# Kernel optimization log

Hardware: AMD Instinct MI355X
Metric: run time of the kernel (lower is better)

Reference implementation:

```python
import math
import jax, jax.numpy as jnp
import numpy as np

NQ, NK = 16384, 4096
QDIM, KDIM, MID = 512, 256, 256


def setup_inputs() -> dict:
    key = jax.random.key(0)
    k1, k2, k3, k4, k5, k6, k7, k8 = jax.random.split(key, 8)
    return {
        "global_embeddings": jax.random.normal(k1, (NQ, QDIM), dtype=jnp.float32),
        "substruct_embeddings": jax.random.normal(k2, (NK, KDIM), dtype=jnp.float32),
        "substruct_weight": jax.random.uniform(k3, (NK,), dtype=jnp.float32),
        "mask": jax.random.randint(k4, (NQ, NK), 0, 2, dtype=jnp.int32),
        "Wq": jax.random.normal(k5, (MID, QDIM), dtype=jnp.float32) / math.sqrt(QDIM),
        "bq": jax.random.normal(k6, (MID,), dtype=jnp.float32) * 0.01,
        "Wk": jax.random.normal(k7, (MID, KDIM), dtype=jnp.float32) / math.sqrt(KDIM),
        "bk": jax.random.normal(k8, (MID,), dtype=jnp.float32) * 0.01,
    }


def reference(global_embeddings, substruct_embeddings, substruct_weight, mask, Wq, bq, Wk, bk):
    # Q/K projections (torch Linear: x @ W.T + b)
    Q = global_embeddings @ Wq.T + bq            # [NQ, MID]
    K = substruct_embeddings @ Wk.T + bk         # [NK, MID]
    scores = (Q @ K.T) / math.sqrt(MID)          # [NQ, NK]
    scores = jnp.where(mask == 0, -jnp.inf, scores)
    attn = jax.nn.softmax(scores, axis=-1)       # row-wise stable softmax
    # torch.diag(w) @ E  ==  elementwise row scaling
    V = substruct_weight[:, None] * substruct_embeddings  # [NK, KDIM]
    return attn @ V                              # [NQ, KDIM]
```

## Files before the change

kernel.cpp:

```cpp
#include <hip/hip_runtime.h>
#include <hip/hip_bf16.h>

typedef __bf16 bf16_t;
typedef bf16_t bf16x8 __attribute__((ext_vector_type(8)));
typedef float  f32x4  __attribute__((ext_vector_type(4)));
typedef unsigned long long u64;
typedef unsigned int u32;

#define MFMA16(A,B,C) __builtin_amdgcn_mfma_f32_16x16x32_bf16((A),(B),(C),0,0,0)


static __device__ __forceinline__ void gl_lds16(const bf16_t* g, void* l) {
    __builtin_amdgcn_global_load_lds(
        (const __attribute__((address_space(1))) u32*)(const void*)g,
        (__attribute__((address_space(3))) u32*)l, 16, 0, 0);
}

template<int KA, bool SWZ>
__global__ __launch_bounds__(256)
void proj_kernel(const float* __restrict__ A, const float* __restrict__ W,
                 const float* __restrict__ b, bf16_t* __restrict__ C,
                 float scale)
{
    __shared__ bf16_t Alds[64][40];
    __shared__ bf16_t Wlds[256][40];

    const int t  = threadIdx.x;
    const int w  = t >> 6, l = t & 63, lr = l & 15, lg = l >> 4;
    const int m0 = blockIdx.x * 64;

    f32x4 acc[16];
#pragma unroll
    for (int tt = 0; tt < 16; ++tt) acc[tt] = (f32x4){0.f, 0.f, 0.f, 0.f};

    const int ar  = t >> 2;
    const int ac8 = (t & 3) * 8;

    for (int kb = 0; kb < KA / 32; ++kb) {
        {
            const float* ap = A + (size_t)(m0 + ar) * KA + kb * 32 + ac8;
            float4 a0 = *(const float4*)ap;
            float4 a1 = *(const float4*)(ap + 4);
            bf16x8 av;
            av[0]=(bf16_t)a0.x; av[1]=(bf16_t)a0.y; av[2]=(bf16_t)a0.z; av[3]=(bf16_t)a0.w;
            av[4]=(bf16_t)a1.x; av[5]=(bf16_t)a1.y; av[6]=(bf16_t)a1.z; av[7]=(bf16_t)a1.w;
            *(bf16x8*)&Alds[ar][ac8] = av;
        }
#pragma unroll
        for (int c = 0; c < 4; ++c) {
            int e8 = c * 256 + t;
            int wr = e8 >> 2, wc8 = (e8 & 3) * 8;
            const float* wp = W + (size_t)wr * KA + kb * 32 + wc8;
            float4 w0 = *(const float4*)wp;
            float4 w1 = *(const float4*)(wp + 4);
            bf16x8 wv;
            wv[0]=(bf16_t)w0.x; wv[1]=(bf16_t)w0.y; wv[2]=(bf16_t)w0.z; wv[3]=(bf16_t)w0.w;
            wv[4]=(bf16_t)w1.x; wv[5]=(bf16_t)w1.y; wv[6]=(bf16_t)w1.z; wv[7]=(bf16_t)w1.w;
            *(bf16x8*)&Wlds[wr][wc8] = wv;
        }
        __syncthreads();

        bf16x8 af = *(bf16x8*)&Alds[w * 16 + lr][lg * 8];
#pragma unroll
        for (int tt = 0; tt < 16; ++tt) {
            bf16x8 bfrag = *(bf16x8*)&Wlds[tt * 16 + lr][lg * 8];
            acc[tt] = MFMA16(af, bfrag, acc[tt]);
        }
        __syncthreads();
    }

#pragma unroll
    for (int tt = 0; tt < 16; ++tt) {
        int col = tt * 16 + lr;
        float bias = b[col];
#pragma unroll
        for (int r = 0; r < 4; ++r) {
            int row = m0 + w * 16 + lg * 4 + r;
            int colS = col;
            if (SWZ) colS = (((col >> 3) ^ (row & 7)) << 3) | (col & 7);
            C[(size_t)row * 256 + colS] = (bf16_t)((acc[tt][r] + bias) * scale);
        }
    }
}

__global__ __launch_bounds__(256)
void buildvt_kernel(const float* __restrict__ S, const float* __restrict__ wgt,
                    bf16_t* __restrict__ VT)
{
    int i = blockIdx.x * 256 + threadIdx.x;
    int d = i >> 12, k = i & 4095;
    int kt = (k & ~63) | (((((k >> 3) & 7) ^ (d & 7)) << 3)) | (k & 7);
    VT[i] = (bf16_t)(wgt[kt] * S[(size_t)kt * 256 + d]);
}

template<bool SPLIT>
__global__ __launch_bounds__(512, 2)
void attn_kernel(const bf16_t* __restrict__ Qb, const bf16_t* __restrict__ Kb,
                 const bf16_t* __restrict__ VT, const int* __restrict__ mask,
                 float* __restrict__ out, float* __restrict__ pacc,
                 float* __restrict__ pm, float* __restrict__ pl)
{
    __shared__ __align__(16) char Kraw[2][32768];
    __shared__ __align__(16) char Vraw[2][32768];
    __shared__ __align__(16) char Praw[16384];

    const int t  = threadIdx.x;
    const int w  = t >> 6, l = t & 63, lr = l & 15, lg = l >> 4;
    const int qw = blockIdx.x * 128 + w * 16;
    const int half = SPLIT ? (int)blockIdx.y : 0;
    const int NT   = SPLIT ? 32 : 64;
    const int kb0  = half * NT;

    bf16x8 qf[8];
    {
        const bf16_t* qrow = Qb + (size_t)(qw + lr) * 256;
#pragma unroll
        for (int kk = 0; kk < 8; ++kk)
            qf[kk] = *(const bf16x8*)(qrow + kk * 32 + lg * 8);
    }

    bf16x8 vone;
#pragma unroll
    for (int j = 0; j < 8; ++j) vone[j] = (bf16_t)1.0f;

    f32x4 acc[16];
#pragma unroll
    for (int dt = 0; dt < 16; ++dt) acc[dt] = (f32x4){0.f, 0.f, 0.f, 0.f};
    f32x4 lacc = (f32x4){0.f, 0.f, 0.f, 0.f};
    float mrow[4];
#pragma unroll
    for (int r = 0; r < 4; ++r) mrow[r] = -1e30f;

    auto stage = [&](int kb, char* kd, char* vd) {
#pragma unroll
        for (int i = 0; i < 4; ++i) {
            int row = w * 8 + i * 2 + (l >> 5);
            gl_lds16(Kb + (size_t)(kb * 64 + row) * 256 + (l & 31) * 8,
                     kd + (w * 8 + i * 2) * 512);
        }
#pragma unroll
        for (int i = 0; i < 4; ++i) {
            int d = w * 32 + i * 8 + (l >> 3);
            gl_lds16(VT + (size_t)d * 4096 + kb * 64 + (l & 7) * 8,
                     vd + (w * 32 + i * 8) * 128);
        }
    };

    auto iter = [&](int kb, char* kcur, char* vcur, char* knxt, char* vnxt,
                    bool do_stage) {
        int4 mv[4];
#pragma unroll
        for (int r = 0; r < 4; ++r)
            mv[r] = *(const int4*)(mask + (size_t)(qw + 4 * lg + r) * 4096
                                   + kb * 64 + lr * 4);

        if (do_stage) stage(kb + 1, knxt, vnxt);

        u64 rowbits[4];
#pragma unroll
        for (int r = 0; r < 4; ++r) {
            u64 b0 = __ballot(mv[r].x != 0);
            u64 b1 = __ballot(mv[r].y != 0);
            u64 b2 = __ballot(mv[r].z != 0);
            u64 b3 = __ballot(mv[r].w != 0);
            u64 w01  = (lr & 1) ? b1 : b0;
            u64 w23  = (lr & 1) ? b3 : b2;
            u64 wsel = (lr & 2) ? w23 : w01;
            rowbits[r] = wsel >> (lg * 16 + (lr >> 2));
        }

        f32x4 s[4];
#pragma unroll
        for (int tt = 0; tt < 4; ++tt) {
            f32x4 sv = (f32x4){0.f, 0.f, 0.f, 0.f};
#pragma unroll
            for (int kk = 0; kk < 8; ++kk) {
                bf16x8 kf = *(bf16x8*)(kcur + (((tt * 16 + lr) * 512)
                                | ((((kk * 4 + lg) ^ (lr & 7)) << 4))));
                sv = MFMA16(qf[kk], kf, sv);
            }
            s[tt] = sv;
        }
#pragma unroll
        for (int tt = 0; tt < 4; ++tt)
#pragma unroll
            for (int r = 0; r < 4; ++r) {
                bool keep = ((rowbits[r] >> (4 * tt)) & 1ull) != 0;
                s[tt][r] = keep ? s[tt][r] : -1e30f;
            }

        float bm[4];
#pragma unroll
        for (int r = 0; r < 4; ++r)
            bm[r] = fmaxf(fmaxf(s[0][r], s[1][r]), fmaxf(s[2][r], s[3][r]));
#pragma unroll
        for (int off = 1; off < 16; off <<= 1)
#pragma unroll
            for (int r = 0; r < 4; ++r)
                bm[r] = fmaxf(bm[r], __shfl_xor(bm[r], off));

        bool need = false;
#pragma unroll
        for (int r = 0; r < 4; ++r) need = need || (bm[r] > mrow[r] + 8.f);
        if (__any(need)) {
#pragma unroll
            for (int r = 0; r < 4; ++r) {
                float mn = fmaxf(mrow[r], bm[r]);
                float fr = __expf(mrow[r] - mn);
                mrow[r] = mn;
                lacc[r] *= fr;
#pragma unroll
                for (int dt = 0; dt < 16; ++dt) acc[dt][r] *= fr;
            }
        }

#pragma unroll
        for (int tt = 0; tt < 4; ++tt)
#pragma unroll
            for (int r = 0; r < 4; ++r) {
                int prow = w * 16 + lg * 4 + r;
                *(bf16_t*)(Praw + ((prow * 128 + (tt * 16 + lr) * 2)
                                   ^ ((prow & 7) << 4)))
                    = (bf16_t)__expf(s[tt][r] - mrow[r]);
            }
        asm volatile("s_waitcnt lgkmcnt(0)" ::: "memory");
        __builtin_amdgcn_sched_barrier(0);

        bf16x8 pa0, pa1;
        {
            int prow = w * 16 + lr;
            pa0 = *(bf16x8*)(Praw + ((prow * 128 + (0 * 4 + lg) * 16)
                                     ^ ((prow & 7) << 4)));
            pa1 = *(bf16x8*)(Praw + ((prow * 128 + (1 * 4 + lg) * 16)
                                     ^ ((prow & 7) << 4)));
        }
        lacc = MFMA16(pa0, vone, lacc);
        lacc = MFMA16(pa1, vone, lacc);
#pragma unroll
        for (int dt = 0; dt < 16; ++dt) {
            int vrow = dt * 16 + lr;
            bf16x8 v0 = *(bf16x8*)(vcur + ((vrow * 128)
                            | ((((0 * 4 + lg) ^ (lr & 7)) << 4))));
            bf16x8 v1 = *(bf16x8*)(vcur + ((vrow * 128)
                            | ((((1 * 4 + lg) ^ (lr & 7)) << 4))));
            acc[dt] = MFMA16(pa0, v0, acc[dt]);
            acc[dt] = MFMA16(pa1, v1, acc[dt]);
        }
        __syncthreads();
    };

    stage(kb0, &Kraw[0][0], &Vraw[0][0]);
    __syncthreads();

    for (int tb = 0; tb < NT; tb += 2) {
        iter(kb0 + tb,     &Kraw[0][0], &Vraw[0][0], &Kraw[1][0], &Vraw[1][0],
             true);
        iter(kb0 + tb + 1, &Kraw[1][0], &Vraw[1][0], &Kraw[0][0], &Vraw[0][0],
             tb + 2 < NT);
    }

    if (SPLIT) {
        float* pa = pacc + (size_t)half * 16384 * 256;
#pragma unroll
        for (int r = 0; r < 4; ++r) {
            int row = qw + lg * 4 + r;
#pragma unroll
            for (int dt = 0; dt < 16; ++dt)
                pa[(size_t)row * 256 + dt * 16 + lr] = acc[dt][r];
            if (lr == 0) {
                pm[half * 16384 + row] = mrow[r];
                pl[half * 16384 + row] = lacc[r];
            }
        }
    } else {
#pragma unroll
        for (int r = 0; r < 4; ++r) {
            float inv = 1.0f / lacc[r];
#pragma unroll
            for (int dt = 0; dt < 16; ++dt)
                out[(size_t)(qw + lg * 4 + r) * 256 + dt * 16 + lr] = acc[dt][r] * inv;
        }
    }
}

__global__ __launch_bounds__(256)
void combine_kernel(const float* __restrict__ pacc, const float* __restrict__ pm,
                    const float* __restrict__ pl, float* __restrict__ out)
{
    int idx = blockIdx.x * 256 + threadIdx.x;
    int row = idx >> 6, c4 = (idx & 63) * 4;
    float m0 = pm[row], m1 = pm[16384 + row];
    float l0 = pl[row], l1 = pl[16384 + row];
    float m  = fmaxf(m0, m1);
    float a  = __expf(m0 - m), b = __expf(m1 - m);
    float inv = 1.0f / (l0 * a + l1 * b);
    float4 x0 = *(const float4*)(pacc + (size_t)row * 256 + c4);
    float4 x1 = *(const float4*)(pacc + (size_t)16384 * 256 + (size_t)row * 256 + c4);
    float4 o;
    o.x = (x0.x * a + x1.x * b) * inv;
    o.y = (x0.y * a + x1.y * b) * inv;
    o.z = (x0.z * a + x1.z * b) * inv;
    o.w = (x0.w * a + x1.w * b) * inv;
    *(float4*)(out + (size_t)row * 256 + c4) = o;
}

extern "C" void kernel_launch(void* const* d_in, const int* in_sizes, int n_in,
                              void* d_out, int out_size, void* d_ws, size_t ws_size,
                              hipStream_t stream)
{
    const float* gE   = (const float*)d_in[0];
    const float* sE   = (const float*)d_in[1];
    const float* wgt  = (const float*)d_in[2];
    const int*   mask = (const int*)  d_in[3];
    const float* Wq   = (const float*)d_in[4];
    const float* bq   = (const float*)d_in[5];
    const float* Wk   = (const float*)d_in[6];
    const float* bk   = (const float*)d_in[7];
    float* out = (float*)d_out;

    char* ws = (char*)d_ws;
    bf16_t* Qb = (bf16_t*)ws;
    bf16_t* Kb = (bf16_t*)(ws + 8388608);
    bf16_t* VT = (bf16_t*)(ws + 10485760);
    float*  pacc = (float*)(ws + 12582912);
    float*  pm   = (float*)(ws + 46137344);
    float*  pl   = (float*)(ws + 46268416);
    const size_t need_full = 46399488;
    const size_t need_min  = 12582912;

    if (ws_size < need_min) return;

    proj_kernel<512, false><<<dim3(256, 1), 256, 0, stream>>>(gE, Wq, bq, Qb, 0.0625f);
    proj_kernel<256, true ><<<dim3(64, 1), 256, 0, stream>>>(sE, Wk, bk, Kb, 1.0f);
    buildvt_kernel<<<4096, 256, 0, stream>>>(sE, wgt, VT);

    if (ws_size >= need_full) {
        attn_kernel<true><<<dim3(128, 2), 512, 0, stream>>>(
            Qb, Kb, VT, mask, out, pacc, pm, pl);
        combine_kernel<<<4096, 256, 0, stream>>>(pacc, pm, pl, out);
    } else {
        attn_kernel<false><<<dim3(128, 1), 512, 0, stream>>>(
            Qb, Kb, VT, mask, out, nullptr, nullptr, nullptr);
    }
}
```

Before: 207.0 us.

## Compute transposed QK^T scores and build P operand in registers instead of LDS

Swaps the MFMA operand order so each lane holds scores for one query row. The row max then needs only two cross-lane shuffles, and the mask can be read directly per lane without ballots. The probability tile is packed to bf16 with v_cvt_pk_bf16_f32 and rearranged into the A-operand layout with permlane32 swaps and xor shuffles, which removes the Praw LDS round trip and its waitcnt. The synchronisation moves to the start of each iteration, replacing the barrier after the initial stage; this adds shuffle work and depends on the lane permutation being correct.

```diff
diff --git a/kernel.cpp b/kernel.cpp
--- a/kernel.cpp
+++ b/kernel.cpp
@@ -102,7 +102,6 @@
 {
     __shared__ __align__(16) char Kraw[2][32768];
     __shared__ __align__(16) char Vraw[2][32768];
-    __shared__ __align__(16) char Praw[16384];
 
     const int t  = threadIdx.x;
     const int w  = t >> 6, l = t & 63, lr = l & 15, lg = l >> 4;
@@ -127,9 +126,7 @@
 #pragma unroll
     for (int dt = 0; dt < 16; ++dt) acc[dt] = (f32x4){0.f, 0.f, 0.f, 0.f};
     f32x4 lacc = (f32x4){0.f, 0.f, 0.f, 0.f};
-    float mrow[4];
-#pragma unroll
-    for (int r = 0; r < 4; ++r) mrow[r] = -1e30f;
+    float mrow = -1e30f;
 
     auto stage = [&](int kb, char* kd, char* vd) {
 #pragma unroll
@@ -150,24 +147,12 @@
                     bool do_stage) {
         int4 mv[4];
 #pragma unroll
-        for (int r = 0; r < 4; ++r)
-            mv[r] = *(const int4*)(mask + (size_t)(qw + 4 * lg + r) * 4096
-                                   + kb * 64 + lr * 4);
+        for (int tt = 0; tt < 4; ++tt)
+            mv[tt] = *(const int4*)(mask + (size_t)(qw + lr) * 4096
+                                    + kb * 64 + tt * 16 + lg * 4);
 
         if (do_stage) stage(kb + 1, knxt, vnxt);
-
-        u64 rowbits[4];
-#pragma unroll
-        for (int r = 0; r < 4; ++r) {
-            u64 b0 = __ballot(mv[r].x != 0);
-            u64 b1 = __ballot(mv[r].y != 0);
-            u64 b2 = __ballot(mv[r].z != 0);
-            u64 b3 = __ballot(mv[r].w != 0);
-            u64 w01  = (lr & 1) ? b1 : b0;
-            u64 w23  = (lr & 1) ? b3 : b2;
-            u64 wsel = (lr & 2) ? w23 : w01;
-            rowbits[r] = wsel >> (lg * 16 + (lr >> 2));
-        }
+        __syncthreads();
 
         f32x4 s[4];
 #pragma unroll
@@ -177,65 +162,85 @@
             for (int kk = 0; kk < 8; ++kk) {
                 bf16x8 kf = *(bf16x8*)(kcur + (((tt * 16 + lr) * 512)
                                 | ((((kk * 4 + lg) ^ (lr & 7)) << 4))));
-                sv = MFMA16(qf[kk], kf, sv);
+                sv = MFMA16(kf, qf[kk], sv);
             }
             s[tt] = sv;
         }
+
+#pragma unroll
+        for (int tt = 0; tt < 4; ++tt) {
+            s[tt][0] = mv[tt].x ? s[tt][0] : -1e30f;
+            s[tt][1] = mv[tt].y ? s[tt][1] : -1e30f;
+            s[tt][2] = mv[tt].z ? s[tt][2] : -1e30f;
+            s[tt][3] = mv[tt].w ? s[tt][3] : -1e30f;
+        }
+
+        float bm;
+        {
+            f32x4 m4 = s[0];
+#pragma unroll
+            for (int tt = 1; tt < 4; ++tt) {
+                m4[0] = fmaxf(m4[0], s[tt][0]);
+                m4[1] = fmaxf(m4[1], s[tt][1]);
+                m4[2] = fmaxf(m4[2], s[tt][2]);
+                m4[3] = fmaxf(m4[3], s[tt][3]);
+            }
+            bm = fmaxf(fmaxf(m4[0], m4[1]), fmaxf(m4[2], m4[3]));
+            bm = fmaxf(bm, __shfl_xor(bm, 16));
+            bm = fmaxf(bm, __shfl_xor(bm, 32));
+        }
+
+        bool need = bm > mrow + 8.f;
+        if (__any(need)) {
+            float mn = fmaxf(mrow, bm);
+            float fr = __expf(mrow - mn);
+            mrow = mn;
+            float frC[4];
+#pragma unroll
+            for (int r = 0; r < 4; ++r) frC[r] = __shfl(fr, lg * 4 + r);
+#pragma unroll
+            for (int r = 0; r < 4; ++r) {
+                lacc[r] *= frC[r];
+#pragma unroll
+                for (int dt = 0; dt < 16; ++dt) acc[dt][r] *= frC[r];
+            }
+        }
+
 #pragma unroll
         for (int tt = 0; tt < 4; ++tt)
 #pragma unroll
-            for (int r = 0; r < 4; ++r) {
-                bool keep = ((rowbits[r] >> (4 * tt)) & 1ull) != 0;
-                s[tt][r] = keep ? s[tt][r] : -1e30f;
-            }
-
-        float bm[4];
-#pragma unroll
-        for (int r = 0; r < 4; ++r)
-            bm[r] = fmaxf(fmaxf(s[0][r], s[1][r]), fmaxf(s[2][r], s[3][r]));
-#pragma unroll
-        for (int off = 1; off < 16; off <<= 1)
-#pragma unroll
             for (int r = 0; r < 4; ++r)
-                bm[r] = fmaxf(bm[r], __shfl_xor(bm[r], off));
-
-        bool need = false;
-#pragma unroll
-        for (int r = 0; r < 4; ++r) need = need || (bm[r] > mrow[r] + 8.f);
-        if (__any(need)) {
-#pragma unroll
-            for (int r = 0; r < 4; ++r) {
-                float mn = fmaxf(mrow[r], bm[r]);
-                float fr = __expf(mrow[r] - mn);
-                mrow[r] = mn;
-                lacc[r] *= fr;
-#pragma unroll
-                for (int dt = 0; dt < 16; ++dt) acc[dt][r] *= fr;
-            }
-        }
-
-#pragma unroll
-        for (int tt = 0; tt < 4; ++tt)
-#pragma unroll
-            for (int r = 0; r < 4; ++r) {
-                int prow = w * 16 + lg * 4 + r;
-                *(bf16_t*)(Praw + ((prow * 128 + (tt * 16 + lr) * 2)
-                                   ^ ((prow & 7) << 4)))
-                    = (bf16_t)__expf(s[tt][r] - mrow[r]);
-            }
-        asm volatile("s_waitcnt lgkmcnt(0)" ::: "memory");
-        __builtin_amdgcn_sched_barrier(0);
-
-        bf16x8 pa0, pa1;
-        {
-            int prow = w * 16 + lr;
-            pa0 = *(bf16x8*)(Praw + ((prow * 128 + (0 * 4 + lg) * 16)
-                                     ^ ((prow & 7) << 4)));
-            pa1 = *(bf16x8*)(Praw + ((prow * 128 + (1 * 4 + lg) * 16)
-                                     ^ ((prow & 7) << 4)));
-        }
-        lacc = MFMA16(pa0, vone, lacc);
-        lacc = MFMA16(pa1, vone, lacc);
+                s[tt][r] = __expf(s[tt][r] - mrow);
+
+        bf16x8 pa[2];
+#pragma unroll
+        for (int g = 0; g < 2; ++g) {
+            u32 x0, x1, y0, y1;
+            asm("v_cvt_pk_bf16_f32 %0, %1, %2"
+                : "=v"(x0) : "v"(s[2 * g][0]), "v"(s[2 * g][1]));
+            asm("v_cvt_pk_bf16_f32 %0, %1, %2"
+                : "=v"(x1) : "v"(s[2 * g][2]), "v"(s[2 * g][3]));
+            asm("v_cvt_pk_bf16_f32 %0, %1, %2"
+                : "=v"(y0) : "v"(s[2 * g + 1][0]), "v"(s[2 * g + 1][1]));
+            asm("v_cvt_pk_bf16_f32 %0, %1, %2"
+                : "=v"(y1) : "v"(s[2 * g + 1][2]), "v"(s[2 * g + 1][3]));
+            asm volatile("v_permlane32_swap_b32 %0, %1" : "+v"(x0), "+v"(y0));
+            asm volatile("v_permlane32_swap_b32 %0, %1" : "+v"(x1), "+v"(y1));
+            u32 sx0 = (u32)__shfl_xor((int)x0, 16);
+            u32 sx1 = (u32)__shfl_xor((int)x1, 16);
+            u32 sy0 = (u32)__shfl_xor((int)y0, 16);
+            u32 sy1 = (u32)__shfl_xor((int)y1, 16);
+            bool evn = (lg & 1) == 0;
+            union { u32 uw[4]; bf16x8 v; } pu;
+            pu.uw[0] = evn ? x0  : sy0;
+            pu.uw[1] = evn ? x1  : sy1;
+            pu.uw[2] = evn ? sx0 : y0;
+            pu.uw[3] = evn ? sx1 : y1;
+            pa[g] = pu.v;
+        }
+
+        lacc = MFMA16(pa[0], vone, lacc);
+        lacc = MFMA16(pa[1], vone, lacc);
 #pragma unroll
         for (int dt = 0; dt < 16; ++dt) {
             int vrow = dt * 16 + lr;
@@ -243,14 +248,13 @@
                             | ((((0 * 4 + lg) ^ (lr & 7)) << 4))));
             bf16x8 v1 = *(bf16x8*)(vcur + ((vrow * 128)
                             | ((((1 * 4 + lg) ^ (lr & 7)) << 4))));
-            acc[dt] = MFMA16(pa0, v0, acc[dt]);
-            acc[dt] = MFMA16(pa1, v1, acc[dt]);
+            acc[dt] = MFMA16(pa[0], v0, acc[dt]);
+            acc[dt] = MFMA16(pa[1], v1, acc[dt]);
         }
         __syncthreads();
     };
 
     stage(kb0, &Kraw[0][0], &Vraw[0][0]);
-    __syncthreads();
 
     for (int tb = 0; tb < NT; tb += 2) {
         iter(kb0 + tb,     &Kraw[0][0], &Vraw[0][0], &Kraw[1][0], &Vraw[1][0],
@@ -260,25 +264,25 @@
     }
 
     if (SPLIT) {
-        float* pa = pacc + (size_t)half * 16384 * 256;
+        float* pa_ = pacc + (size_t)half * 16384 * 256;
 #pragma unroll
         for (int r = 0; r < 4; ++r) {
             int row = qw + lg * 4 + r;
 #pragma unroll
             for (int dt = 0; dt < 16; ++dt)
-                pa[(size_t)row * 256 + dt * 16 + lr] = acc[dt][r];
-            if (lr == 0) {
-                pm[half * 16384 + row] = mrow[r];
-                pl[half * 16384 + row] = lacc[r];
-            }
-        }
+                pa_[(size_t)row * 256 + dt * 16 + lr] = acc[dt][r];
+            if (lr == 0) pl[half * 16384 + row] = lacc[r];
+        }
+        if (lg == 0 && (w == (l >> 4) || true))
+            pm[half * 16384 + qw + lr] = mrow;
     } else {
 #pragma unroll
         for (int r = 0; r < 4; ++r) {
             float inv = 1.0f / lacc[r];
 #pragma unroll
             for (int dt = 0; dt < 16; ++dt)
-                out[(size_t)(qw + lg * 4 + r) * 256 + dt * 16 + lr] = acc[dt][r] * inv;
+                out[(size_t)(qw + lg * 4 + r) * 256 + dt * 16 + lr]
+                    = acc[dt][r] * inv;
         }
     }
 }
```

Measured after the change: 215.8 us. 1.04x slower.
